# Kernel tuning notes

Measured on AMD Instinct MI355X. Metric: run time of the kernel, lower is better.

The kernel has to match this reference:

```python
import jax, jax.numpy as jnp
import numpy as np
from jax import lax

FEAT_STRIDE = 16
PRE_NMS_TOP_N = 6000   # cfg['TEST'].RPN_PRE_NMS_TOP_N
POST_NMS_TOP_N = 300   # cfg['TEST'].RPN_POST_NMS_TOP_N
NMS_THRESH = 0.7       # cfg['TEST'].RPN_NMS_THRESH
NUM_ANCHORS = 9        # len(scales) * len(ratios)


def _whctrs(a):
    w = a[2] - a[0] + 1.0
    h = a[3] - a[1] + 1.0
    return w, h, a[0] + 0.5 * (w - 1), a[1] + 0.5 * (h - 1)


def _mkanchors(ws, hs, xc, yc):
    ws = np.asarray(ws, dtype=np.float64)[:, None]
    hs = np.asarray(hs, dtype=np.float64)[:, None]
    return np.hstack([xc - 0.5 * (ws - 1), yc - 0.5 * (hs - 1),
                      xc + 0.5 * (ws - 1), yc + 0.5 * (hs - 1)])


def generate_anchors(base_size=16, ratios=np.array([0.5, 1.0, 2.0]), scales=np.array([8, 16, 32])):
    base = np.array([1, 1, base_size, base_size], dtype=np.float64) - 1
    w, h, xc, yc = _whctrs(base)
    size = w * h
    ws = np.round(np.sqrt(size / ratios))
    hs = np.round(ws * ratios)
    ratio_anchors = _mkanchors(ws, hs, xc, yc)
    out = []
    for a in ratio_anchors:
        aw, ah, axc, ayc = _whctrs(a)
        out.append(_mkanchors(aw * scales, ah * scales, axc, ayc))
    return np.vstack(out).astype(np.float32)


ANCHORS = jnp.asarray(generate_anchors())  # (A, 4)


def _bbox_transform_inv(boxes, deltas):
    widths = boxes[:, 2] - boxes[:, 0] + 1.0
    heights = boxes[:, 3] - boxes[:, 1] + 1.0
    ctr_x = boxes[:, 0] + 0.5 * widths
    ctr_y = boxes[:, 1] + 0.5 * heights
    dx, dy, dw, dh = deltas[:, 0], deltas[:, 1], deltas[:, 2], deltas[:, 3]
    pcx = dx * widths + ctr_x
    pcy = dy * heights + ctr_y
    pw = jnp.exp(dw) * widths
    ph = jnp.exp(dh) * heights
    return jnp.stack([pcx - 0.5 * pw, pcy - 0.5 * ph,
                      pcx + 0.5 * pw, pcy + 0.5 * ph], axis=1)


def _clip_boxes(boxes, im_info):
    # im_info = [im_h, im_w, scale]
    return jnp.stack([
        jnp.clip(boxes[:, 0], 0.0, im_info[1] - 1.0),
        jnp.clip(boxes[:, 1], 0.0, im_info[0] - 1.0),
        jnp.clip(boxes[:, 2], 0.0, im_info[1] - 1.0),
        jnp.clip(boxes[:, 3], 0.0, im_info[0] - 1.0)], axis=1)


def _nms_keep(boxes, thresh):
    # Greedy NMS over score-sorted boxes via precomputed pairwise IoU + scan.
    x1, y1, x2, y2 = boxes[:, 0], boxes[:, 1], boxes[:, 2], boxes[:, 3]
    areas = (x2 - x1 + 1.0) * (y2 - y1 + 1.0)
    iw = jnp.maximum(jnp.minimum(x2[:, None], x2[None, :]) - jnp.maximum(x1[:, None], x1[None, :]) + 1.0, 0.0)
    ih = jnp.maximum(jnp.minimum(y2[:, None], y2[None, :]) - jnp.maximum(y1[:, None], y1[None, :]) + 1.0, 0.0)
    inter = iw * ih
    iou = inter / (areas[:, None] + areas[None, :] - inter)  # (N, N)
    n = boxes.shape[0]
    ids = jnp.arange(n)

    def step(supp, xs):
        row, i = xs
        keep_i = jnp.logical_not(supp[i])
        supp = supp | (keep_i & (row > thresh) & (ids > i))
        return supp, keep_i

    _, keep = lax.scan(step, jnp.zeros((n,), dtype=bool), (iou, ids))
    return keep


def setup_inputs() -> dict:
    H = W = 100
    k1, k2 = jax.random.split(jax.random.key(0))
    scores = jax.random.uniform(k1, (1, 2 * NUM_ANCHORS, H, W), dtype=jnp.float32)
    bbox_delta = jax.random.normal(k2, (1, 4 * NUM_ANCHORS, H, W), dtype=jnp.float32) * 0.1
    im_info = jnp.array([H * FEAT_STRIDE, W * FEAT_STRIDE, 1.0], dtype=jnp.float32)
    return {"scores": scores, "bbox_delta": bbox_delta, "im_info": im_info, "cfg_key": 0}


def reference(scores, bbox_delta, im_info, cfg_key):
    A = NUM_ANCHORS
    fg = scores[:, A:, :, :]                         # (1, A, H, W) fg scores
    H, W = fg.shape[2], fg.shape[3]
    sx = (jnp.arange(W) * FEAT_STRIDE).astype(jnp.float32)
    sy = (jnp.arange(H) * FEAT_STRIDE).astype(jnp.float32)
    gx, gy = jnp.meshgrid(sx, sy)                    # 'xy' indexing -> (H, W)
    shifts = jnp.stack([gx.ravel(), gy.ravel(), gx.ravel(), gy.ravel()], axis=1)  # (K, 4)
    anchors = (ANCHORS[None, :, :] + shifts[:, None, :]).reshape(-1, 4)           # (K*A, 4)

    deltas = bbox_delta.transpose(0, 2, 3, 1).reshape(-1, 4)
    proposals = _clip_boxes(_bbox_transform_inv(anchors, deltas), im_info)

    sc = fg.transpose(0, 2, 3, 1).reshape(-1)        # (K*A,)
    _, order = lax.top_k(sc, PRE_NMS_TOP_N)          # sort desc + pre-NMS top-N
    props = proposals[order]                         # (PRE, 4)

    keep = _nms_keep(props, NMS_THRESH)              # (PRE,) bool, score order preserved
    rank = jnp.cumsum(keep) - 1
    valid = keep & (rank < POST_NMS_TOP_N)
    idx = jnp.where(valid, rank, POST_NMS_TOP_N)     # invalid rows -> scratch slot
    rows = jnp.concatenate([jnp.zeros((props.shape[0], 1), props.dtype), props], axis=1)
    rows = rows * valid[:, None]
    output = jnp.zeros((POST_NMS_TOP_N + 1, 5), props.dtype).at[idx].set(rows)[:POST_NMS_TOP_N]
    return output, anchors
```

## Files before the change

### kernel.cpp

```cpp
#include <hip/hip_runtime.h>
#include <hip/hip_bf16.h>


#define W100 100
#define HW10K 10000
#define NANCH 90000
#define PRE_TOPN 6000
#define POST_TOPN 300
#define PADN 8192
#define NLIST 8
#define LISTN 1024
#define NWORD 94
#define NMS_TH 0.7f
#define NHB 22

typedef unsigned long long u64;
typedef unsigned u32;

__constant__ float c_anch[9][4] = {
    {-84.f,  -40.f,  99.f,  55.f},
    {-176.f, -88.f,  191.f, 103.f},
    {-360.f, -184.f, 375.f, 199.f},
    {-56.f,  -56.f,  71.f,  71.f},
    {-120.f, -120.f, 135.f, 135.f},
    {-248.f, -248.f, 263.f, 263.f},
    {-36.f,  -80.f,  51.f,  95.f},
    {-80.f,  -168.f, 95.f,  183.f},
    {-168.f, -344.f, 183.f, 359.f}
};


__global__ __launch_bounds__(1024)
void k_prep(float4* __restrict__ anc_out, u32* __restrict__ hist,
            u32* __restrict__ meta, float* __restrict__ out) {
    const int gtid = (int)blockIdx.x * 1024 + threadIdx.x;
    if (gtid < 8192) hist[gtid] = 0u;
    if (gtid < POST_TOPN * 5) out[gtid] = 0.f;
    if (gtid < 8) meta[gtid] = 0u;
    if (gtid >= NANCH) return;
    int a = gtid % 9, pos = gtid / 9;
    int y = pos / W100, x = pos - y * W100;
    float sx = (float)(x * 16), sy = (float)(y * 16);
    anc_out[gtid] = make_float4(c_anch[a][0] + sx, c_anch[a][1] + sy,
                                c_anch[a][2] + sx, c_anch[a][3] + sy);
}

__global__ __launch_bounds__(1024)
void k_hist(const float* __restrict__ scores, u32* __restrict__ hist,
            u32* __restrict__ meta) {
    __shared__ u32 lh[8192];
    __shared__ u32 wsum_s[16], wtail_s[16];
    __shared__ int s_last;
    const int tid = threadIdx.x;
    const int gtid = (int)blockIdx.x * 1024 + tid;

    for (int i = tid; i < 8192; i += 1024) lh[i] = 0u;
    __syncthreads();
    const float4* fg4 = (const float4*)(scores + 9 * HW10K);
    if (gtid < 22500) {
        float4 v = fg4[gtid];
        atomicAdd(&lh[__float_as_uint(v.x) >> 17], 1u);
        atomicAdd(&lh[__float_as_uint(v.y) >> 17], 1u);
        atomicAdd(&lh[__float_as_uint(v.z) >> 17], 1u);
        atomicAdd(&lh[__float_as_uint(v.w) >> 17], 1u);
    }
    __syncthreads();
    for (int i = tid; i < 8192; i += 1024) {
        u32 c = lh[i];
        if (c) atomicAdd(&hist[i], c);
    }
    __syncthreads();
    if (tid == 0) {
        u32 r = __hip_atomic_fetch_add(&meta[6], 1u, __ATOMIC_ACQ_REL,
                                       __HIP_MEMORY_SCOPE_AGENT);
        s_last = (r == (u32)NHB - 1u);
    }
    __syncthreads();
    if (!s_last) return;
    __builtin_amdgcn_fence(__ATOMIC_ACQUIRE, "agent");

    const int w = tid >> 6, lane = tid & 63;
    u32 h[8];
#pragma unroll
    for (int b = 0; b < 8; ++b)
        h[b] = __hip_atomic_load(&hist[tid * 8 + b], __ATOMIC_RELAXED,
                                 __HIP_MEMORY_SCOPE_AGENT);
    u32 gs = h[0] + h[1] + h[2] + h[3] + h[4] + h[5] + h[6] + h[7];
    u32 suf = gs;
#pragma unroll
    for (int d = 1; d < 64; d <<= 1) {
        u32 t = (u32)__shfl((int)suf, (lane + d) & 63);
        suf += (lane + d < 64) ? t : 0u;
    }
    if (lane == 0) wsum_s[w] = suf;
    __syncthreads();
    if (w == 0) {
        u32 v = (lane < 16) ? wsum_s[lane] : 0u;
        u32 s2 = v;
#pragma unroll
        for (int d = 1; d < 16; d <<= 1) {
            u32 t = (u32)__shfl((int)s2, (lane + d) & 63);
            s2 += (lane + d < 16) ? t : 0u;
        }
        if (lane < 16) wtail_s[lane] = s2 - v;
    }
    __syncthreads();
    u32 S = suf + wtail_s[w];
    if (S >= (u32)PRE_TOPN && S - gs < (u32)PRE_TOPN) {
        u32 run = S - gs;
        u32 T = (u32)tid * 8u;
        for (int b = 7; b >= 0; --b) {
            run += h[b];
            if (run >= (u32)PRE_TOPN) { T = (u32)tid * 8u + (u32)b; break; }
        }
        __hip_atomic_store(&meta[1], T << 17, __ATOMIC_RELAXED,
                           __HIP_MEMORY_SCOPE_AGENT);
    }
}

__global__ __launch_bounds__(1024)
void k_csort(const float* __restrict__ scores, u64* __restrict__ keys,
             const u32* __restrict__ meta) {
    __shared__ u64 s[LISTN];
    __shared__ u32 s_cnt;
    const int tid = threadIdx.x;
    const int gtid = (int)blockIdx.x * 1024 + tid;

    for (int i = tid; i < LISTN; i += 1024) s[i] = 0ull;
    if (tid == 0) s_cnt = 0u;
    const u32 thr = meta[1];
    __syncthreads();

    const float4* fg4 = (const float4*)(scores + 9 * HW10K);
    for (int i4 = gtid; i4 < 22500; i4 += 8192) {
        float4 v = fg4[i4];
        float sv[4] = {v.x, v.y, v.z, v.w};
#pragma unroll
        for (int e = 0; e < 4; ++e) {
            int f = 4 * i4 + e;
            u32 bits = __float_as_uint(sv[e]);
            if (bits >= thr) {
                int a = f / HW10K, pos = f - a * HW10K;
                u32 idx = (u32)(pos * 9 + a);
                u32 slot = atomicAdd(&s_cnt, 1u);
                if (slot < (u32)LISTN)
                    s[slot] = ((u64)bits << 32) | (u32)(~idx);
            }
        }
    }
    __syncthreads();

    for (u32 k = 2; k <= (u32)LISTN; k <<= 1) {
        for (u32 j = k >> 1; j > 0; j >>= 1) {
            if (tid < 512) {
                u32 p  = (u32)tid;
                u32 i  = 2u * p - (p & (j - 1u));
                u32 ix = i | j;
                u64 A = s[i], B = s[ix];
                bool asc = (i & k) != 0u;
                bool sw  = asc ? (A > B) : (A < B);
                if (sw) { s[i] = B; s[ix] = A; }
            }
            __syncthreads();
        }
    }
    u64* seg = keys + (size_t)blockIdx.x * LISTN;
    for (int i = tid; i < LISTN; i += 1024) seg[i] = s[i];
}

__global__ __launch_bounds__(1024)
void k_rankdec(const u64* __restrict__ keys, const float* __restrict__ bbox,
               const float* __restrict__ im_info, float4* __restrict__ boxes) {
    __shared__ u64 lk[PADN];
    const int tid = threadIdx.x;
    const int gtid = (int)blockIdx.x * 1024 + tid;
    for (int i = tid; i < PADN; i += 1024) lk[i] = keys[i];
    __syncthreads();

    const u64 e = lk[gtid];
    if (e == 0ull) return;
    const int l = (int)blockIdx.x;
    int rank = tid;
#pragma unroll
    for (int l2 = 0; l2 < NLIST; ++l2) {
        if (l2 == l) continue;
        const u64* lst = lk + (size_t)l2 * LISTN;
        int lo = 0, hi = LISTN;
        while (lo < hi) {
            int mid = (lo + hi) >> 1;
            if (lst[mid] > e) lo = mid + 1; else hi = mid;
        }
        rank += lo;
    }
    if (rank >= PRE_TOPN) return;

    const u32 idx = ~((u32)e);
    int pos = (int)(idx / 9u);
    int a   = (int)(idx - (u32)pos * 9u);
    int y = pos / W100, x = pos - y * W100;
    float sx = (float)(x * 16), sy = (float)(y * 16);
    float ax1 = c_anch[a][0] + sx, ay1 = c_anch[a][1] + sy;
    float ax2 = c_anch[a][2] + sx, ay2 = c_anch[a][3] + sy;
    float w = ax2 - ax1 + 1.f, h = ay2 - ay1 + 1.f;
    float cx = ax1 + 0.5f * w,  cy = ay1 + 0.5f * h;
    float dx = bbox[(a * 4 + 0) * HW10K + pos];
    float dy = bbox[(a * 4 + 1) * HW10K + pos];
    float dw = bbox[(a * 4 + 2) * HW10K + pos];
    float dh = bbox[(a * 4 + 3) * HW10K + pos];
    float pcx = dx * w + cx, pcy = dy * h + cy;
    float pw = expf(dw) * w, ph = expf(dh) * h;
    float imH = im_info[0], imW = im_info[1];
    float x1 = pcx - 0.5f * pw, y1 = pcy - 0.5f * ph;
    float x2 = pcx + 0.5f * pw, y2 = pcy + 0.5f * ph;
    x1 = fminf(fmaxf(x1, 0.f), imW - 1.f);
    x2 = fminf(fmaxf(x2, 0.f), imW - 1.f);
    y1 = fminf(fmaxf(y1, 0.f), imH - 1.f);
    y2 = fminf(fmaxf(y2, 0.f), imH - 1.f);
    boxes[rank] = make_float4(x1, y1, x2, y2);
}

__global__ __launch_bounds__(64)
void k_iou(const float4* __restrict__ bx, u64* __restrict__ M) {
    const int rb = blockIdx.y, cb = blockIdx.x;
    if (cb < rb) return;
    __shared__ float4 cbox[64];
    const int tid = threadIdx.x;
    const int col0 = cb * 64;
    {
        int cj = col0 + tid;
        cbox[tid] = (cj < PRE_TOPN) ? bx[cj] : make_float4(0.f, 0.f, -2.f, -2.f);
    }
    __syncthreads();
    const int ri = rb * 64 + tid;
    if (ri >= PRE_TOPN) return;
    float4 b = bx[ri];
    float area = (b.z - b.x + 1.f) * (b.w - b.y + 1.f);
    u64 bits = 0ull;
    const int ncol = (col0 + 64 <= PRE_TOPN) ? 64 : (PRE_TOPN - col0);
#pragma unroll 8
    for (int k = 0; k < 64; ++k) {
        if (k >= ncol) break;
        float4 q = cbox[k];
        float qa = (q.z - q.x + 1.f) * (q.w - q.y + 1.f);
        float iw = fmaxf(fminf(b.z, q.z) - fmaxf(b.x, q.x) + 1.f, 0.f);
        float ih = fmaxf(fminf(b.w, q.w) - fmaxf(b.y, q.y) + 1.f, 0.f);
        float inter = iw * ih;
        float iou = inter / ((area + qa) - inter);
        if ((col0 + k > ri) && (iou > NMS_TH)) bits |= (1ull << k);
    }
    M[(size_t)ri * NWORD + cb] = bits;
}

__global__ __launch_bounds__(1024)
void k_scan(const u64* __restrict__ M, const float4* __restrict__ bx,
            float* __restrict__ out) {
    __shared__ u64 s_diag[2][64];
    __shared__ u64 s_supp[2];
    __shared__ u64 s_keptc;
    __shared__ int K[384];
    __shared__ int s_nK, s_nK2, s_rank;
    const int tid = threadIdx.x;
    const int lane = tid & 63;

    if (tid < 64) s_diag[0][tid] = M[(size_t)tid * NWORD + 0];
    if (tid == 0) { s_supp[0] = 0ull; s_supp[1] = 0ull; s_nK = 0; s_rank = 0; }
    __syncthreads();

    for (int c = 0; c < NWORD; ++c) {
        const int par = c & 1, nxt = par ^ 1;
        const int w1 = c + 1;
        const int nK0 = s_nK;
        u64 kval = 0ull, cval = 0ull, dval = 0ull;
        if (w1 < NWORD) {
            if (tid < nK0) {
                kval = M[(size_t)K[tid] * NWORD + w1];
            } else if (tid >= 512 && tid < 576) {
                int j2 = w1 * 64 + (tid - 512);
                if (j2 < PRE_TOPN) dval = M[(size_t)j2 * NWORD + w1];
            } else if (tid >= 576 && tid < 640) {
                int j3 = c * 64 + (tid - 576);
                if (j3 < PRE_TOPN) cval = M[(size_t)j3 * NWORD + w1];
            }
        }
        if (tid < 64) {
            const int j = c * 64 + tid;
            const bool valid = j < PRE_TOPN;
            u64 m = s_diag[par][tid];
            u64 alive = __ballot(valid) & ~s_supp[par];
            u64 kept = 0ull;
            while (alive) {
                int k = (int)__builtin_ctzll(alive);
                kept |= (1ull << k);
                u32 mlo = (u32)__builtin_amdgcn_readlane((int)(u32)m, k);
                u32 mhi = (u32)__builtin_amdgcn_readlane((int)(u32)(m >> 32), k);
                alive &= ~(((u64)mhi << 32) | mlo);
                alive &= ~(1ull << k);
            }
            int r0 = s_rank;
            if ((kept >> tid) & 1ull) {
                int rin = (int)__popcll(kept & ((1ull << tid) - 1ull));
                K[nK0 + rin] = j;
                int r = r0 + rin;
                if (r < POST_TOPN) {
                    float4 b = bx[j];
                    out[r * 5 + 0] = 0.f;
                    out[r * 5 + 1] = b.x; out[r * 5 + 2] = b.y;
                    out[r * 5 + 3] = b.z; out[r * 5 + 4] = b.w;
                }
            }
            if (tid == 0) {
                int nk = (int)__popcll(kept);
                s_keptc = kept;
                s_nK2 = nK0 + nk;
                s_rank = r0 + nk;
            }
        }
        __syncthreads();
        if (s_rank >= POST_TOPN || w1 >= NWORD) break;
        if (tid == 0) { s_supp[par] = 0ull; s_nK = s_nK2; }
        u64 v = (tid < nK0) ? kval : 0ull;
        if (tid >= 576 && tid < 640 && ((s_keptc >> (tid - 576)) & 1ull)) v |= cval;
        v |= __shfl_xor((unsigned long long)v, 1);
        v |= __shfl_xor((unsigned long long)v, 2);
        v |= __shfl_xor((unsigned long long)v, 4);
        v |= __shfl_xor((unsigned long long)v, 8);
        v |= __shfl_xor((unsigned long long)v, 16);
        v |= __shfl_xor((unsigned long long)v, 32);
        if (lane == 0 && v) atomicOr(&s_supp[nxt], v);
        if (tid >= 512 && tid < 576) s_diag[nxt][tid - 512] = dval;
        __syncthreads();
    }
}

extern "C" void kernel_launch(void* const* d_in, const int* in_sizes, int n_in,
                              void* d_out, int out_size, void* d_ws, size_t ws_size,
                              hipStream_t stream) {
    const float* scores  = (const float*)d_in[0];
    const float* bbox    = (const float*)d_in[1];
    const float* im_info = (const float*)d_in[2];
    float* out = (float*)d_out;

    u64*    keys  = (u64*)d_ws;
    float4* boxes = (float4*)((char*)d_ws + PADN * sizeof(u64));
    u32*    meta  = (u32*)((char*)d_ws + 161536);
    u32*    hist  = (u32*)((char*)d_ws + 163840);
    u64*    M     = (u64*)((char*)d_ws + 196608);
    float4* anc   = (float4*)(out + POST_TOPN * 5);

    k_prep  <<<88, 1024, 0, stream>>>(anc, hist, meta, out);
    k_hist  <<<NHB, 1024, 0, stream>>>(scores, hist, meta);
    k_csort <<<NLIST, 1024, 0, stream>>>(scores, keys, meta);
    k_rankdec<<<NLIST, 1024, 0, stream>>>(keys, bbox, im_info, boxes);
    dim3 g(NWORD, NWORD);
    k_iou   <<<g, 64, 0, stream>>>(boxes, M);
    k_scan  <<<1, 1024, 0, stream>>>(M, boxes, out);
}
```

Before: 78.30 us.

## Use register shuffle bitonic sort and fold anchor generation into idle IoU blocks

Rewrites the per-list bitonic sort to keep one key per thread in registers, using wavefront shuffles for strides under 64 and shared memory only for larger strides. This cuts shared-memory traffic and the number of block barriers. Anchor generation moves into the otherwise idle lower-triangle blocks of the IoU kernel, and output zeroing moves into the scan kernel, so the prep kernel becomes much smaller. The risk is that the larger-stride steps keep their barrier round trips, and the IoU kernel now carries some extra store work.

After: 81.07 us. 3.5% more time.

```diff
diff --git a/kernel.cpp b/kernel.cpp
--- a/kernel.cpp
+++ b/kernel.cpp
@@ -31,18 +31,10 @@
 
 
 __global__ __launch_bounds__(1024)
-void k_prep(float4* __restrict__ anc_out, u32* __restrict__ hist,
-            u32* __restrict__ meta, float* __restrict__ out) {
+void k_prep(u32* __restrict__ hist, u32* __restrict__ meta) {
     const int gtid = (int)blockIdx.x * 1024 + threadIdx.x;
     if (gtid < 8192) hist[gtid] = 0u;
-    if (gtid < POST_TOPN * 5) out[gtid] = 0.f;
     if (gtid < 8) meta[gtid] = 0u;
-    if (gtid >= NANCH) return;
-    int a = gtid % 9, pos = gtid / 9;
-    int y = pos / W100, x = pos - y * W100;
-    float sx = (float)(x * 16), sy = (float)(y * 16);
-    anc_out[gtid] = make_float4(c_anch[a][0] + sx, c_anch[a][1] + sy,
-                                c_anch[a][2] + sx, c_anch[a][3] + sy);
 }
 
 __global__ __launch_bounds__(1024)
@@ -150,22 +142,33 @@
     }
     __syncthreads();
 
-    for (u32 k = 2; k <= (u32)LISTN; k <<= 1) {
+    u64 K = s[tid];
+#pragma unroll
+    for (u32 k = 2; k <= 64; k <<= 1) {
         for (u32 j = k >> 1; j > 0; j >>= 1) {
-            if (tid < 512) {
-                u32 p  = (u32)tid;
-                u32 i  = 2u * p - (p & (j - 1u));
-                u32 ix = i | j;
-                u64 A = s[i], B = s[ix];
-                bool asc = (i & k) != 0u;
-                bool sw  = asc ? (A > B) : (A < B);
-                if (sw) { s[i] = B; s[ix] = A; }
-            }
+            u64 Kp = __shfl_xor((unsigned long long)K, (int)j);
+            bool sel = (((u32)tid & k) != 0u) ^ (((u32)tid & j) != 0u);
+            K = sel ? (K < Kp ? K : Kp) : (K > Kp ? K : Kp);
+        }
+    }
+    for (u32 k = 128; k <= 1024; k <<= 1) {
+        for (u32 j = k >> 1; j >= 64; j >>= 1) {
             __syncthreads();
+            s[tid] = K;
+            __syncthreads();
+            u64 Kp = s[tid ^ (int)j];
+            bool sel = (((u32)tid & k) != 0u) ^ (((u32)tid & j) != 0u);
+            K = sel ? (K < Kp ? K : Kp) : (K > Kp ? K : Kp);
+        }
+#pragma unroll
+        for (u32 j = 32; j > 0; j >>= 1) {
+            u64 Kp = __shfl_xor((unsigned long long)K, (int)j);
+            bool sel = (((u32)tid & k) != 0u) ^ (((u32)tid & j) != 0u);
+            K = sel ? (K < Kp ? K : Kp) : (K > Kp ? K : Kp);
         }
     }
     u64* seg = keys + (size_t)blockIdx.x * LISTN;
-    for (int i = tid; i < LISTN; i += 1024) seg[i] = s[i];
+    seg[tid] = K;
 }
 
 __global__ __launch_bounds__(1024)
@@ -220,11 +223,23 @@
 }
 
 __global__ __launch_bounds__(64)
-void k_iou(const float4* __restrict__ bx, u64* __restrict__ M) {
+void k_iou(const float4* __restrict__ bx, u64* __restrict__ M,
+           float4* __restrict__ anc_out) {
     const int rb = blockIdx.y, cb = blockIdx.x;
-    if (cb < rb) return;
+    const int tid = threadIdx.x;
+    if (cb < rb) {
+        int lid = ((rb * (rb - 1)) >> 1) + cb;
+        int idx = lid * 64 + tid;
+        if (idx < NANCH) {
+            int a = idx % 9, pos = idx / 9;
+            int y = pos / W100, x = pos - y * W100;
+            float sx = (float)(x * 16), sy = (float)(y * 16);
+            anc_out[idx] = make_float4(c_anch[a][0] + sx, c_anch[a][1] + sy,
+                                       c_anch[a][2] + sx, c_anch[a][3] + sy);
+        }
+        return;
+    }
     __shared__ float4 cbox[64];
-    const int tid = threadIdx.x;
     const int col0 = cb * 64;
     {
         int cj = col0 + tid;
@@ -262,6 +277,7 @@
     const int tid = threadIdx.x;
     const int lane = tid & 63;
 
+    for (int i = tid; i < POST_TOPN * 5; i += 1024) out[i] = 0.f;
     if (tid < 64) s_diag[0][tid] = M[(size_t)tid * NWORD + 0];
     if (tid == 0) { s_supp[0] = 0ull; s_supp[1] = 0ull; s_nK = 0; s_rank = 0; }
     __syncthreads();
@@ -347,11 +363,11 @@
     u64*    M     = (u64*)((char*)d_ws + 196608);
     float4* anc   = (float4*)(out + POST_TOPN * 5);
 
-    k_prep  <<<88, 1024, 0, stream>>>(anc, hist, meta, out);
+    k_prep  <<<8, 1024, 0, stream>>>(hist, meta);
     k_hist  <<<NHB, 1024, 0, stream>>>(scores, hist, meta);
     k_csort <<<NLIST, 1024, 0, stream>>>(scores, keys, meta);
     k_rankdec<<<NLIST, 1024, 0, stream>>>(keys, bbox, im_info, boxes);
     dim3 g(NWORD, NWORD);
-    k_iou   <<<g, 64, 0, stream>>>(boxes, M);
+    k_iou   <<<g, 64, 0, stream>>>(boxes, M, anc);
     k_scan  <<<1, 1024, 0, stream>>>(M, boxes, out);
 }
```
